# Kernel optimization log

Measured on AMD Instinct MI355X. Metric: run time of the kernel, lower is better.

The kernel has to match this reference:

```python
import jax, jax.numpy as jnp
import numpy as np

N = 50000      # nodes
E = 800000     # edges (avg degree 16)
EMB = 128      # emb_dim
NF = 7         # x_features
EF = 5         # edge_features
L = 5          # num_layer
BN_EPS = 1e-5


def setup_inputs() -> dict:
    key = jax.random.key(0)
    ks = jax.random.split(key, 12)
    s = 0.05
    return {
        "x": jax.random.normal(ks[0], (N, NF), jnp.float32),
        "edge_attr": jax.random.normal(ks[1], (E, EF), jnp.float32),
        "edge_index": jax.random.randint(ks[2], (2, E), 0, N, dtype=jnp.int32),
        "W_x": jax.random.normal(ks[3], (NF, EMB), jnp.float32) * s,
        "b_x": jax.random.normal(ks[4], (NF, EMB), jnp.float32) * s,
        "W_e": jax.random.normal(ks[5], (L, EF, EMB), jnp.float32) * s,
        "b_e": jax.random.normal(ks[6], (L, EF, EMB), jnp.float32) * s,
        # per-layer GIN update MLP: Linear(EMB,2EMB)-ReLU-Linear(2EMB,EMB)
        "W1": jax.random.normal(ks[7], (L, EMB, 2 * EMB), jnp.float32) * s,
        "b1": jnp.zeros((L, 2 * EMB), jnp.float32),
        "W2": jax.random.normal(ks[8], (L, 2 * EMB, EMB), jnp.float32) * s,
        "b2": jnp.zeros((L, EMB), jnp.float32),
        # per-layer BatchNorm1d affine params
        "gamma": jnp.ones((L, EMB), jnp.float32),
        "beta": jnp.zeros((L, EMB), jnp.float32),
    }


def reference(x, edge_attr, W_x, b_x, W_e, b_e, W1, b1, W2, b2, gamma, beta, edge_index):
    src, dst = edge_index[0], edge_index[1]
    # initial node embedding: sum of 7 Linear(1,EMB) applied per column == x @ W_x + sum(biases)
    h = x @ W_x + b_x.sum(axis=0)  # [N, EMB]
    for l in range(L):
        # edge embeddings: sum of EF Linear(1,EMB) over edge_attr columns
        e_emb = edge_attr @ W_e[l] + b_e[l].sum(axis=0)  # [E, EMB]
        sl_emb = b_e[l].sum(axis=0)  # self-loop edges have zero attr -> bias sum
        # message = x_j + edge_emb, aggr = add (scatter over dst); self loops add h + sl_emb
        msg = h[src] + e_emb                                        # [E, EMB]
        agg = jax.ops.segment_sum(msg, dst, num_segments=N) + h + sl_emb  # [N, EMB]
        # GIN update MLP
        z = jax.nn.relu(agg @ W1[l] + b1[l]) @ W2[l] + b2[l]        # [N, EMB]
        # BatchNorm1d (training-mode batch stats, biased variance)
        mu = z.mean(axis=0)
        var = z.var(axis=0)
        z = (z - mu) * jax.lax.rsqrt(var + BN_EPS) * gamma[l] + beta[l]
        # ELU on all but last layer; dropout is identity at drop_ratio=0; JK='last'
        h = jax.nn.elu(z) if l < L - 1 else z
    return h
```

## Files before the change

kernel.cpp:

```cpp
#include <hip/hip_runtime.h>
#include <math.h>

#define NN 50000
#define NE 800000
#define EMB 128
#define HID 256
#define NF 7
#define EF 5
#define NL 5
#define BN_EPS 1e-5f
#define NREP 32
#define SCAN_B 196

typedef _Float16 f16x8 __attribute__((ext_vector_type(8)));
typedef __attribute__((ext_vector_type(4))) float f32x4;

__device__ inline unsigned pkh2(float a, float b) {
    union { unsigned v; _Float16 h[2]; } x;
    x.h[0] = (_Float16)a; x.h[1] = (_Float16)b;
    return x.v;
}
__device__ inline float2 uph2(unsigned u) {
    union { unsigned v; _Float16 h[2]; } x; x.v = u;
    return make_float2((float)x.h[0], (float)x.h[1]);
}
__device__ inline unsigned short f2h_bits(float f) {
    _Float16 h = (_Float16)f;
    return __builtin_bit_cast(unsigned short, h);
}
__device__ inline float h_bits2f(unsigned short b) {
    return (float)__builtin_bit_cast(_Float16, b);
}

__global__ void k_prep(const float* __restrict__ b_x, const float* __restrict__ b_e,
                       float* __restrict__ bsum_x, float* __restrict__ bsum_e,
                       int* __restrict__ counts, int* __restrict__ cursor) {
    int tid = threadIdx.x;
    if (blockIdx.x == 0 && tid < EMB) {
        float s = 0.f;
        for (int f = 0; f < NF; ++f) s += b_x[f * EMB + tid];
        bsum_x[tid] = s;
        for (int l = 0; l < NL; ++l) {
            float se = 0.f;
            for (int f = 0; f < EF; ++f) se += b_e[(l * EF + f) * EMB + tid];
            bsum_e[l * EMB + tid] = se;
        }
    }
    int gid = blockIdx.x * blockDim.x + tid;
    int stride = gridDim.x * blockDim.x;
    for (int i = gid; i < NN; i += stride) { counts[i] = 0; cursor[i] = 0; }
}

__global__ void k_prepw(const float* __restrict__ W1, const float* __restrict__ W2,
                        unsigned short* __restrict__ W1ph, unsigned short* __restrict__ W1pl,
                        unsigned short* __restrict__ W2ph, unsigned short* __restrict__ W2pl) {
    const int TOT = NL * EMB * HID;
    int gid = blockIdx.x * blockDim.x + threadIdx.x;
    if (gid < TOT) {
        int l = gid / (EMB * HID);
        int r = gid % (EMB * HID);
        int w = r >> 13;
        int rem = r & 8191;
        int h2 = rem >> 11;
        int rem2 = rem & 2047;
        int kk = rem2 >> 9;
        int rem3 = rem2 & 511;
        int lane = rem3 >> 3;
        int j = rem3 & 7;
        int hc = w * 64 + h2 * 16 + (lane & 15);
        int k = kk * 32 + (lane >> 4) * 8 + j;
        float wv = W1[((size_t)l * EMB + k) * HID + hc];
        unsigned short hi = f2h_bits(wv);
        W1ph[gid] = hi;
        W1pl[gid] = f2h_bits(wv - h_bits2f(hi));
    } else if (gid < 2 * TOT) {
        int g = gid - TOT;
        int l = g / (EMB * HID);
        int r = g % (EMB * HID);
        int w = r >> 13;
        int rem = r & 8191;
        int o2 = rem >> 12;
        int rem2 = rem & 4095;
        int kk = rem2 >> 9;
        int rem3 = rem2 & 511;
        int lane = rem3 >> 3;
        int j = rem3 & 7;
        int oc = w * 32 + o2 * 16 + (lane & 15);
        int k2 = kk * 32 + (lane >> 4) * 8 + j;
        float wv = W2[((size_t)l * HID + k2) * EMB + oc];
        unsigned short hi = f2h_bits(wv);
        W2ph[g] = hi;
        W2pl[g] = f2h_bits(wv - h_bits2f(hi));
    }
}

__global__ void k_init(const float* __restrict__ x, const float* __restrict__ W_x,
                       const float* __restrict__ bsum_x, unsigned short* __restrict__ h16) {
    int gid = blockIdx.x * blockDim.x + threadIdx.x;
    int v = gid >> 5;
    if (v >= NN) return;
    int c = (gid & 31) << 2;
    float4 acc = *(const float4*)(bsum_x + c);
    #pragma unroll
    for (int f = 0; f < NF; ++f) {
        float xv = x[(size_t)v * NF + f];
        float4 w = *(const float4*)(W_x + f * EMB + c);
        acc.x += xv * w.x; acc.y += xv * w.y; acc.z += xv * w.z; acc.w += xv * w.w;
    }
    uint2 p = make_uint2(pkh2(acc.x, acc.y), pkh2(acc.z, acc.w));
    *(uint2*)(h16 + (size_t)v * EMB + c) = p;
}

__global__ void k_hist(const int* __restrict__ dst, int* __restrict__ counts) {
    int e = blockIdx.x * blockDim.x + threadIdx.x;
    if (e < NE) atomicAdd(&counts[dst[e]], 1);
}

__global__ void k_scan1(const int* __restrict__ counts, int* __restrict__ bsum) {
    int tid = threadIdx.x;
    int i = blockIdx.x * 256 + tid;
    int v = (i < NN) ? counts[i] : 0;
    #pragma unroll
    for (int off = 1; off < 64; off <<= 1) v += __shfl_xor(v, off, 64);
    __shared__ int ws[4];
    if ((tid & 63) == 0) ws[tid >> 6] = v;
    __syncthreads();
    if (tid == 0) bsum[blockIdx.x] = ws[0] + ws[1] + ws[2] + ws[3];
}

__global__ void k_scan2(const int* __restrict__ bsum, int* __restrict__ bpre,
                        int* __restrict__ row_start) {
    int tid = threadIdx.x;
    int x = (tid < SCAN_B) ? bsum[tid] : 0;
    int lane = tid & 63, wv = tid >> 6;
    int v = x;
    #pragma unroll
    for (int off = 1; off < 64; off <<= 1) {
        int t = __shfl_up(v, off, 64);
        if (lane >= off) v += t;
    }
    __shared__ int wsum[4];
    if (lane == 63) wsum[wv] = v;
    __syncthreads();
    int woff = 0;
    #pragma unroll
    for (int w = 0; w < 4; ++w) if (w < wv) woff += wsum[w];
    int incl = v + woff;
    if (tid < SCAN_B) bpre[tid] = incl - x;
    if (tid == 255) row_start[NN] = incl;
}

__global__ void k_scan3(const int* __restrict__ counts, const int* __restrict__ bpre,
                        int* __restrict__ row_start) {
    int tid = threadIdx.x;
    int i = blockIdx.x * 256 + tid;
    int x = (i < NN) ? counts[i] : 0;
    int lane = tid & 63, wv = tid >> 6;
    int v = x;
    #pragma unroll
    for (int off = 1; off < 64; off <<= 1) {
        int t = __shfl_up(v, off, 64);
        if (lane >= off) v += t;
    }
    __shared__ int wsum[4];
    if (lane == 63) wsum[wv] = v;
    __syncthreads();
    int woff = 0;
    #pragma unroll
    for (int w = 0; w < 4; ++w) if (w < wv) woff += wsum[w];
    if (i < NN) row_start[i] = bpre[blockIdx.x] + v + woff - x;
}

__global__ void k_fill(const int* __restrict__ src, const int* __restrict__ dst,
                       const float* __restrict__ edge_attr,
                       const int* __restrict__ row_start, int* __restrict__ cursor,
                       uint4* __restrict__ sorted_pk) {
    int e = blockIdx.x * blockDim.x + threadIdx.x;
    if (e >= NE) return;
    int d = dst[e];
    int pos = atomicAdd(&cursor[d], 1);
    int idx = row_start[d] + pos;
    const float* ea = edge_attr + (size_t)e * EF;
    float a0 = ea[0], a1 = ea[1], a2 = ea[2], a3 = ea[3], a4 = ea[4];
    uint4 pk;
    pk.x = (unsigned)src[e];
    pk.y = pkh2(a0, a1);
    pk.z = pkh2(a2, a3);
    pk.w = pkh2(a4, 0.f);
    sorted_pk[idx] = pk;
}

__global__ void k_esum(const uint4* __restrict__ sorted_pk,
                       const int* __restrict__ row_start,
                       float* __restrict__ attsum, int* __restrict__ sorted_srcc) {
    int v = blockIdx.x * blockDim.x + threadIdx.x;
    if (v >= NN) return;
    int e0 = row_start[v], e1 = row_start[v + 1];
    float s0 = 0.f, s1 = 0.f, s2 = 0.f, s3 = 0.f, s4 = 0.f;
    for (int e = e0; e < e1; ++e) {
        uint4 pk = sorted_pk[e];
        sorted_srcc[e] = (int)pk.x;
        float2 a01 = uph2(pk.y), a23 = uph2(pk.z), a4x = uph2(pk.w);
        s0 += a01.x; s1 += a01.y; s2 += a23.x; s3 += a23.y; s4 += a4x.x;
    }
    float* o = attsum + (size_t)v * 8;
    *(float4*)(o) = make_float4(s0, s1, s2, s3);
    *(float4*)(o + 4) = make_float4(s4, (float)(e1 - e0), 0.f, 0.f);
}

template<int APPLY_BN>
__global__ __launch_bounds__(256) void k_agg(
        const unsigned short* __restrict__ st16, const int* __restrict__ sorted_srcc,
        const float* __restrict__ attsum, const float* __restrict__ scsh,
        const float* __restrict__ W_e_l, const float* __restrict__ bsum_e_l,
        const int* __restrict__ row_start,
        unsigned short* __restrict__ agg16, float* __restrict__ stats) {
    int tid = threadIdx.x;
    if (blockIdx.x < NREP) stats[blockIdx.x * 2 * EMB + tid] = 0.f;
    int gid = blockIdx.x * 256 + tid;
    int v = gid >> 6;
    if (v >= NN) return;
    int c = (gid & 63) << 1;
    float2 we0 = *(const float2*)(W_e_l + 0 * EMB + c);
    float2 we1 = *(const float2*)(W_e_l + 1 * EMB + c);
    float2 we2 = *(const float2*)(W_e_l + 2 * EMB + c);
    float2 we3 = *(const float2*)(W_e_l + 3 * EMB + c);
    float2 we4 = *(const float2*)(W_e_l + 4 * EMB + c);
    float2 bs = *(const float2*)(bsum_e_l + c);
    float2 sc2 = make_float2(0.f, 0.f), sh2 = make_float2(0.f, 0.f);
    if (APPLY_BN) {
        sc2 = *(const float2*)(scsh + c);
        sh2 = *(const float2*)(scsh + EMB + c);
    }
    auto state = [&](unsigned u) -> float2 {
        float2 t = uph2(u);
        if (APPLY_BN) {
            t.x = t.x * sc2.x + sh2.x;
            t.y = t.y * sc2.y + sh2.y;
            t.x = (t.x > 0.f) ? t.x : (__expf(t.x) - 1.f);
            t.y = (t.y > 0.f) ? t.y : (__expf(t.y) - 1.f);
        }
        return t;
    };
    float2 hv = state(*(const unsigned*)(st16 + (size_t)v * EMB + c));
    const float* at = attsum + (size_t)v * 8;
    float4 a03 = *(const float4*)(at);
    float2 a45 = *(const float2*)(at + 4);
    float ax = hv.x + (a45.y + 1.f) * bs.x
             + a03.x*we0.x + a03.y*we1.x + a03.z*we2.x + a03.w*we3.x + a45.x*we4.x;
    float ay = hv.y + (a45.y + 1.f) * bs.y
             + a03.x*we0.y + a03.y*we1.y + a03.z*we2.y + a03.w*we3.y + a45.x*we4.y;
    int e0 = row_start[v], e1 = row_start[v + 1];
    int e = e0;
    for (; e + 8 <= e1; e += 8) {
        int s0 = __builtin_amdgcn_readfirstlane(sorted_srcc[e + 0]);
        int s1 = __builtin_amdgcn_readfirstlane(sorted_srcc[e + 1]);
        int s2 = __builtin_amdgcn_readfirstlane(sorted_srcc[e + 2]);
        int s3 = __builtin_amdgcn_readfirstlane(sorted_srcc[e + 3]);
        int s4 = __builtin_amdgcn_readfirstlane(sorted_srcc[e + 4]);
        int s5 = __builtin_amdgcn_readfirstlane(sorted_srcc[e + 5]);
        int s6 = __builtin_amdgcn_readfirstlane(sorted_srcc[e + 6]);
        int s7 = __builtin_amdgcn_readfirstlane(sorted_srcc[e + 7]);
        unsigned u0 = *(const unsigned*)(st16 + (size_t)s0 * EMB + c);
        unsigned u1 = *(const unsigned*)(st16 + (size_t)s1 * EMB + c);
        unsigned u2 = *(const unsigned*)(st16 + (size_t)s2 * EMB + c);
        unsigned u3 = *(const unsigned*)(st16 + (size_t)s3 * EMB + c);
        unsigned u4 = *(const unsigned*)(st16 + (size_t)s4 * EMB + c);
        unsigned u5 = *(const unsigned*)(st16 + (size_t)s5 * EMB + c);
        unsigned u6 = *(const unsigned*)(st16 + (size_t)s6 * EMB + c);
        unsigned u7 = *(const unsigned*)(st16 + (size_t)s7 * EMB + c);
        float2 h0 = state(u0), h1 = state(u1), h2 = state(u2), h3 = state(u3);
        float2 h4 = state(u4), h5 = state(u5), h6 = state(u6), h7 = state(u7);
        ax += ((h0.x + h1.x) + (h2.x + h3.x)) + ((h4.x + h5.x) + (h6.x + h7.x));
        ay += ((h0.y + h1.y) + (h2.y + h3.y)) + ((h4.y + h5.y) + (h6.y + h7.y));
    }
    for (; e < e1; ++e) {
        int s = __builtin_amdgcn_readfirstlane(sorted_srcc[e]);
        float2 hs = state(*(const unsigned*)(st16 + (size_t)s * EMB + c));
        ax += hs.x;
        ay += hs.y;
    }
    *(unsigned*)(agg16 + (size_t)v * EMB + c) = pkh2(ax, ay);
}

__global__ __launch_bounds__(256) void k_mlp(
        const unsigned short* __restrict__ agg16,
        const unsigned short* __restrict__ W1ph, const unsigned short* __restrict__ W1pl,
        const float* __restrict__ b1_l,
        const unsigned short* __restrict__ W2ph, const unsigned short* __restrict__ W2pl,
        const float* __restrict__ b2_l,
        unsigned short* __restrict__ z16, float* __restrict__ stats) {
    __shared__ unsigned short A16[32][136];
    __shared__ unsigned short Hid16[32][264];
    int tid = threadIdx.x;
    int r0 = blockIdx.x * 32;
    int rep = blockIdx.x & (NREP - 1);
    #pragma unroll
    for (int it = 0; it < 2; ++it) {
        int idx = it * 256 + tid;
        int row = idx >> 4;
        int cb = (idx & 15) * 8;
        int grow = r0 + row;
        uint4 val = make_uint4(0u, 0u, 0u, 0u);
        if (grow < NN) val = *(const uint4*)(agg16 + (size_t)grow * EMB + cb);
        *(uint4*)(&A16[row][cb]) = val;
    }
    __syncthreads();
    int wave = tid >> 6, lane = tid & 63;
    int l16 = lane & 15, quad = lane >> 4;
    {
        f16x8 af[2][4];
        #pragma unroll
        for (int nt = 0; nt < 2; ++nt)
            #pragma unroll
            for (int kk = 0; kk < 4; ++kk)
                af[nt][kk] = *(const f16x8*)(&A16[nt * 16 + l16][kk * 32 + quad * 8]);
        #pragma unroll
        for (int h2 = 0; h2 < 4; ++h2) {
            f16x8 whf[4], wlf[4];
            #pragma unroll
            for (int kk = 0; kk < 4; ++kk) {
                size_t off = ((((size_t)(wave * 4 + h2) * 4) + kk) * 64 + lane) * 8;
                whf[kk] = *(const f16x8*)(W1ph + off);
                wlf[kk] = *(const f16x8*)(W1pl + off);
            }
            float4 bv = *(const float4*)(b1_l + wave * 64 + h2 * 16 + quad * 4);
            f32x4 bias = {bv.x, bv.y, bv.z, bv.w};
            #pragma unroll
            for (int nt = 0; nt < 2; ++nt) {
                f32x4 acc = bias;
                #pragma unroll
                for (int kk = 0; kk < 4; ++kk)
                    acc = __builtin_amdgcn_mfma_f32_16x16x32_f16(whf[kk], af[nt][kk], acc, 0, 0, 0);
                #pragma unroll
                for (int kk = 0; kk < 4; ++kk)
                    acc = __builtin_amdgcn_mfma_f32_16x16x32_f16(wlf[kk], af[nt][kk], acc, 0, 0, 0);
                uint2 p;
                p.x = pkh2(fmaxf(acc[0], 0.f), fmaxf(acc[1], 0.f));
                p.y = pkh2(fmaxf(acc[2], 0.f), fmaxf(acc[3], 0.f));
                int col = wave * 64 + h2 * 16 + quad * 4;
                *(uint2*)(&Hid16[nt * 16 + l16][col]) = p;
            }
        }
    }
    __syncthreads();
    float ss[2][4] = {}, sq[2][4] = {};
    #pragma unroll
    for (int o2 = 0; o2 < 2; ++o2) {
        f16x8 w2h[8], w2l[8];
        #pragma unroll
        for (int kk = 0; kk < 8; ++kk) {
            size_t off = ((((size_t)(wave * 2 + o2) * 8) + kk) * 64 + lane) * 8;
            w2h[kk] = *(const f16x8*)(W2ph + off);
            w2l[kk] = *(const f16x8*)(W2pl + off);
        }
        float4 bv = *(const float4*)(b2_l + wave * 32 + o2 * 16 + quad * 4);
        f32x4 bias = {bv.x, bv.y, bv.z, bv.w};
        #pragma unroll
        for (int nt = 0; nt < 2; ++nt) {
            f16x8 hf[8];
            #pragma unroll
            for (int kk = 0; kk < 8; ++kk)
                hf[kk] = *(const f16x8*)(&Hid16[nt * 16 + l16][kk * 32 + quad * 8]);
            f32x4 acc = bias;
            #pragma unroll
            for (int kk = 0; kk < 8; ++kk)
                acc = __builtin_amdgcn_mfma_f32_16x16x32_f16(w2h[kk], hf[kk], acc, 0, 0, 0);
            #pragma unroll
            for (int kk = 0; kk < 8; ++kk)
                acc = __builtin_amdgcn_mfma_f32_16x16x32_f16(w2l[kk], hf[kk], acc, 0, 0, 0);
            int node = r0 + nt * 16 + l16;
            if (node < NN) {
                uint2 p = make_uint2(pkh2(acc[0], acc[1]), pkh2(acc[2], acc[3]));
                *(uint2*)(z16 + (size_t)node * EMB + wave * 32 + o2 * 16 + quad * 4) = p;
                #pragma unroll
                for (int r = 0; r < 4; ++r) {
                    ss[o2][r] += acc[r];
                    sq[o2][r] += acc[r] * acc[r];
                }
            }
        }
    }
    #pragma unroll
    for (int o2 = 0; o2 < 2; ++o2)
        #pragma unroll
        for (int r = 0; r < 4; ++r) {
            float s = ss[o2][r], q = sq[o2][r];
            #pragma unroll
            for (int m = 1; m < 16; m <<= 1) {
                s += __shfl_xor(s, m, 64);
                q += __shfl_xor(q, m, 64);
            }
            if (l16 == 0) {
                int oc = wave * 32 + o2 * 16 + quad * 4 + r;
                atomicAdd(&stats[rep * 2 * EMB + oc], s);
                atomicAdd(&stats[rep * 2 * EMB + EMB + oc], q);
            }
        }
}

__global__ void k_bnscale(const float* __restrict__ stats,
                          const float* __restrict__ gamma_l, const float* __restrict__ beta_l,
                          float* __restrict__ scsh) {
    int tid = threadIdx.x;
    float s = 0.f, q = 0.f;
    #pragma unroll
    for (int r = 0; r < NREP; ++r) {
        s += stats[r * 2 * EMB + tid];
        q += stats[r * 2 * EMB + EMB + tid];
    }
    float mu = s * (1.f / NN);
    float var = q * (1.f / NN) - mu * mu;
    float sf = gamma_l[tid] * rsqrtf(var + BN_EPS);
    scsh[tid] = sf;
    scsh[EMB + tid] = beta_l[tid] - mu * sf;
}

__global__ void k_bn(const unsigned short* __restrict__ z16, const float* __restrict__ scsh,
                     float* __restrict__ fout) {
    __shared__ float sc[EMB], sh[EMB];
    int tid = threadIdx.x;
    if (tid < EMB) {
        sc[tid] = scsh[tid];
        sh[tid] = scsh[EMB + tid];
    }
    __syncthreads();
    int gid = blockIdx.x * blockDim.x + tid;
    if (gid >= NN * EMB / 4) return;
    int c = (gid & 31) << 2;
    uint2 zp = *(const uint2*)(z16 + (size_t)gid * 4);
    float2 z01 = uph2(zp.x), z23 = uph2(zp.y);
    float o0 = z01.x * sc[c + 0] + sh[c + 0];
    float o1 = z01.y * sc[c + 1] + sh[c + 1];
    float o2 = z23.x * sc[c + 2] + sh[c + 2];
    float o3 = z23.y * sc[c + 3] + sh[c + 3];
    *(float4*)(fout + (size_t)gid * 4) = make_float4(o0, o1, o2, o3);
}

extern "C" void kernel_launch(void* const* d_in, const int* in_sizes, int n_in,
                              void* d_out, int out_size, void* d_ws, size_t ws_size,
                              hipStream_t stream) {
    const float* x         = (const float*)d_in[0];
    const float* edge_attr = (const float*)d_in[1];
    const int*   edge_idx  = (const int*)d_in[2];
    const float* W_x   = (const float*)d_in[3];
    const float* b_x   = (const float*)d_in[4];
    const float* W_e   = (const float*)d_in[5];
    const float* b_e   = (const float*)d_in[6];
    const float* W1    = (const float*)d_in[7];
    const float* b1    = (const float*)d_in[8];
    const float* W2    = (const float*)d_in[9];
    const float* b2    = (const float*)d_in[10];
    const float* gamma = (const float*)d_in[11];
    const float* beta  = (const float*)d_in[12];
    float* fout = (float*)d_out;

    const int* src = edge_idx;
    const int* dst = edge_idx + NE;

    char* p = (char*)d_ws;
    auto alloc = [&](size_t bytes) { char* q = p; p += (bytes + 255) & ~(size_t)255; return q; };
    unsigned short* h16  = (unsigned short*)alloc((size_t)NN * EMB * 2);
    unsigned short* z16  = (unsigned short*)alloc((size_t)NN * EMB * 2);
    unsigned short* agg16 = (unsigned short*)alloc((size_t)NN * EMB * 2);
    unsigned short* W1ph = (unsigned short*)alloc((size_t)NL * HID * EMB * 2);
    unsigned short* W1pl = (unsigned short*)alloc((size_t)NL * HID * EMB * 2);
    unsigned short* W2ph = (unsigned short*)alloc((size_t)NL * EMB * HID * 2);
    unsigned short* W2pl = (unsigned short*)alloc((size_t)NL * EMB * HID * 2);
    int*   row_start  = (int*)alloc((NN + 1) * sizeof(int));
    int*   counts     = (int*)alloc(NN * sizeof(int));
    int*   cursor     = (int*)alloc(NN * sizeof(int));
    uint4* sorted_pk  = (uint4*)alloc((size_t)NE * sizeof(uint4));
    int*   sorted_srcc= (int*)alloc((size_t)NE * sizeof(int));
    float* attsum     = (float*)alloc((size_t)NN * 8 * sizeof(float));
    int*   bsum       = (int*)alloc(SCAN_B * sizeof(int));
    int*   bpre       = (int*)alloc(SCAN_B * sizeof(int));
    float* stats      = (float*)alloc((size_t)NREP * 2 * EMB * sizeof(float));
    float* scsh       = (float*)alloc(2 * EMB * sizeof(float));
    float* bsum_x     = (float*)alloc(EMB * sizeof(float));
    float* bsum_e     = (float*)alloc(NL * EMB * sizeof(float));

    k_prep<<<256, 256, 0, stream>>>(b_x, b_e, bsum_x, bsum_e, counts, cursor);
    k_prepw<<<(2 * NL * EMB * HID + 255) / 256, 256, 0, stream>>>(W1, W2, W1ph, W1pl, W2ph, W2pl);
    k_init<<<(NN * 32 + 255) / 256, 256, 0, stream>>>(x, W_x, bsum_x, h16);
    k_hist<<<(NE + 255) / 256, 256, 0, stream>>>(dst, counts);
    k_scan1<<<SCAN_B, 256, 0, stream>>>(counts, bsum);
    k_scan2<<<1, 256, 0, stream>>>(bsum, bpre, row_start);
    k_scan3<<<SCAN_B, 256, 0, stream>>>(counts, bpre, row_start);
    k_fill<<<(NE + 255) / 256, 256, 0, stream>>>(src, dst, edge_attr, row_start, cursor,
                                                 sorted_pk);
    k_esum<<<SCAN_B, 256, 0, stream>>>(sorted_pk, row_start, attsum, sorted_srcc);
    const int AGG_GRID = (NN * 64 + 255) / 256;
    for (int l = 0; l < NL; ++l) {
        if (l == 0) {
            k_agg<0><<<AGG_GRID, 256, 0, stream>>>(
                h16, sorted_srcc, attsum, scsh,
                W_e + (size_t)l * EF * EMB, bsum_e + l * EMB, row_start,
                agg16, stats);
        } else {
            k_agg<1><<<AGG_GRID, 256, 0, stream>>>(
                z16, sorted_srcc, attsum, scsh,
                W_e + (size_t)l * EF * EMB, bsum_e + l * EMB, row_start,
                agg16, stats);
        }
        k_mlp<<<(NN + 31) / 32, 256, 0, stream>>>(
            agg16,
            W1ph + (size_t)l * HID * EMB, W1pl + (size_t)l * HID * EMB, b1 + (size_t)l * HID,
            W2ph + (size_t)l * EMB * HID, W2pl + (size_t)l * EMB * HID, b2 + (size_t)l * EMB,
            z16, stats);
        k_bnscale<<<1, 128, 0, stream>>>(stats, gamma + l * EMB, beta + l * EMB, scsh);
    }
    k_bn<<<(NN * EMB / 4 + 255) / 256, 256, 0, stream>>>(z16, scsh, fout);
}
```

Before: 617.7 us.

## Materialize BN+ELU state once per layer and sum neighbors in packed fp16

Instead of applying batch-norm scale/shift and ELU to every gathered neighbor in the aggregation kernel, a per-layer k_bn pass now writes the normalized, activated state to an fp16 buffer that the next aggregation gathers directly. Groups of eight neighbor rows are also summed with packed half-precision adds before being added to the fp32 accumulator. This removes redundant per-edge exp and FMA work. In exchange it adds an extra elementwise pass and extra memory traffic per layer, and it lowers accumulation precision.

```diff
diff --git a/kernel.cpp b/kernel.cpp
--- a/kernel.cpp
+++ b/kernel.cpp
@@ -13,6 +13,7 @@
 #define SCAN_B 196
 
 typedef _Float16 f16x8 __attribute__((ext_vector_type(8)));
+typedef _Float16 f16x2 __attribute__((ext_vector_type(2)));
 typedef __attribute__((ext_vector_type(4))) float f32x4;
 
 __device__ inline unsigned pkh2(float a, float b) {
@@ -31,6 +32,7 @@
 __device__ inline float h_bits2f(unsigned short b) {
     return (float)__builtin_bit_cast(_Float16, b);
 }
+__device__ inline f16x2 as_h2(unsigned u) { return __builtin_bit_cast(f16x2, u); }
 
 __global__ void k_prep(const float* __restrict__ b_x, const float* __restrict__ b_e,
                        float* __restrict__ bsum_x, float* __restrict__ bsum_e,
@@ -208,10 +210,9 @@
     *(float4*)(o + 4) = make_float4(s4, (float)(e1 - e0), 0.f, 0.f);
 }
 
-template<int APPLY_BN>
 __global__ __launch_bounds__(256) void k_agg(
-        const unsigned short* __restrict__ st16, const int* __restrict__ sorted_srcc,
-        const float* __restrict__ attsum, const float* __restrict__ scsh,
+        const unsigned short* __restrict__ h16, const int* __restrict__ sorted_srcc,
+        const float* __restrict__ attsum,
         const float* __restrict__ W_e_l, const float* __restrict__ bsum_e_l,
         const int* __restrict__ row_start,
         unsigned short* __restrict__ agg16, float* __restrict__ stats) {
@@ -227,22 +228,7 @@
     float2 we3 = *(const float2*)(W_e_l + 3 * EMB + c);
     float2 we4 = *(const float2*)(W_e_l + 4 * EMB + c);
     float2 bs = *(const float2*)(bsum_e_l + c);
-    float2 sc2 = make_float2(0.f, 0.f), sh2 = make_float2(0.f, 0.f);
-    if (APPLY_BN) {
-        sc2 = *(const float2*)(scsh + c);
-        sh2 = *(const float2*)(scsh + EMB + c);
-    }
-    auto state = [&](unsigned u) -> float2 {
-        float2 t = uph2(u);
-        if (APPLY_BN) {
-            t.x = t.x * sc2.x + sh2.x;
-            t.y = t.y * sc2.y + sh2.y;
-            t.x = (t.x > 0.f) ? t.x : (__expf(t.x) - 1.f);
-            t.y = (t.y > 0.f) ? t.y : (__expf(t.y) - 1.f);
-        }
-        return t;
-    };
-    float2 hv = state(*(const unsigned*)(st16 + (size_t)v * EMB + c));
+    float2 hv = uph2(*(const unsigned*)(h16 + (size_t)v * EMB + c));
     const float* at = attsum + (size_t)v * 8;
     float4 a03 = *(const float4*)(at);
     float2 a45 = *(const float2*)(at + 4);
@@ -261,22 +247,27 @@
         int s5 = __builtin_amdgcn_readfirstlane(sorted_srcc[e + 5]);
         int s6 = __builtin_amdgcn_readfirstlane(sorted_srcc[e + 6]);
         int s7 = __builtin_amdgcn_readfirstlane(sorted_srcc[e + 7]);
-        unsigned u0 = *(const unsigned*)(st16 + (size_t)s0 * EMB + c);
-        unsigned u1 = *(const unsigned*)(st16 + (size_t)s1 * EMB + c);
-        unsigned u2 = *(const unsigned*)(st16 + (size_t)s2 * EMB + c);
-        unsigned u3 = *(const unsigned*)(st16 + (size_t)s3 * EMB + c);
-        unsigned u4 = *(const unsigned*)(st16 + (size_t)s4 * EMB + c);
-        unsigned u5 = *(const unsigned*)(st16 + (size_t)s5 * EMB + c);
-        unsigned u6 = *(const unsigned*)(st16 + (size_t)s6 * EMB + c);
-        unsigned u7 = *(const unsigned*)(st16 + (size_t)s7 * EMB + c);
-        float2 h0 = state(u0), h1 = state(u1), h2 = state(u2), h3 = state(u3);
-        float2 h4 = state(u4), h5 = state(u5), h6 = state(u6), h7 = state(u7);
-        ax += ((h0.x + h1.x) + (h2.x + h3.x)) + ((h4.x + h5.x) + (h6.x + h7.x));
-        ay += ((h0.y + h1.y) + (h2.y + h3.y)) + ((h4.y + h5.y) + (h6.y + h7.y));
+        unsigned u0 = *(const unsigned*)(h16 + (size_t)s0 * EMB + c);
+        unsigned u1 = *(const unsigned*)(h16 + (size_t)s1 * EMB + c);
+        unsigned u2 = *(const unsigned*)(h16 + (size_t)s2 * EMB + c);
+        unsigned u3 = *(const unsigned*)(h16 + (size_t)s3 * EMB + c);
+        unsigned u4 = *(const unsigned*)(h16 + (size_t)s4 * EMB + c);
+        unsigned u5 = *(const unsigned*)(h16 + (size_t)s5 * EMB + c);
+        unsigned u6 = *(const unsigned*)(h16 + (size_t)s6 * EMB + c);
+        unsigned u7 = *(const unsigned*)(h16 + (size_t)s7 * EMB + c);
+        f16x2 p01 = as_h2(u0) + as_h2(u1);
+        f16x2 p23 = as_h2(u2) + as_h2(u3);
+        f16x2 p45 = as_h2(u4) + as_h2(u5);
+        f16x2 p67 = as_h2(u6) + as_h2(u7);
+        f16x2 p03 = p01 + p23;
+        f16x2 p47 = p45 + p67;
+        f16x2 p07 = p03 + p47;
+        ax += (float)p07.x;
+        ay += (float)p07.y;
     }
     for (; e < e1; ++e) {
         int s = __builtin_amdgcn_readfirstlane(sorted_srcc[e]);
-        float2 hs = state(*(const unsigned*)(st16 + (size_t)s * EMB + c));
+        float2 hs = uph2(*(const unsigned*)(h16 + (size_t)s * EMB + c));
         ax += hs.x;
         ay += hs.y;
     }
@@ -417,7 +408,7 @@
 }
 
 __global__ void k_bn(const unsigned short* __restrict__ z16, const float* __restrict__ scsh,
-                     float* __restrict__ fout) {
+                     unsigned short* __restrict__ h16, float* __restrict__ fout, int last) {
     __shared__ float sc[EMB], sh[EMB];
     int tid = threadIdx.x;
     if (tid < EMB) {
@@ -434,7 +425,16 @@
     float o1 = z01.y * sc[c + 1] + sh[c + 1];
     float o2 = z23.x * sc[c + 2] + sh[c + 2];
     float o3 = z23.y * sc[c + 3] + sh[c + 3];
-    *(float4*)(fout + (size_t)gid * 4) = make_float4(o0, o1, o2, o3);
+    if (!last) {
+        o0 = (o0 > 0.f) ? o0 : (__expf(o0) - 1.f);
+        o1 = (o1 > 0.f) ? o1 : (__expf(o1) - 1.f);
+        o2 = (o2 > 0.f) ? o2 : (__expf(o2) - 1.f);
+        o3 = (o3 > 0.f) ? o3 : (__expf(o3) - 1.f);
+        uint2 p = make_uint2(pkh2(o0, o1), pkh2(o2, o3));
+        *(uint2*)(h16 + (size_t)gid * 4) = p;
+    } else {
+        *(float4*)(fout + (size_t)gid * 4) = make_float4(o0, o1, o2, o3);
+    }
 }
 
 extern "C" void kernel_launch(void* const* d_in, const int* in_sizes, int n_in,
@@ -492,23 +492,17 @@
     k_esum<<<SCAN_B, 256, 0, stream>>>(sorted_pk, row_start, attsum, sorted_srcc);
     const int AGG_GRID = (NN * 64 + 255) / 256;
     for (int l = 0; l < NL; ++l) {
-        if (l == 0) {
-            k_agg<0><<<AGG_GRID, 256, 0, stream>>>(
-                h16, sorted_srcc, attsum, scsh,
-                W_e + (size_t)l * EF * EMB, bsum_e + l * EMB, row_start,
-                agg16, stats);
-        } else {
-            k_agg<1><<<AGG_GRID, 256, 0, stream>>>(
-                z16, sorted_srcc, attsum, scsh,
-                W_e + (size_t)l * EF * EMB, bsum_e + l * EMB, row_start,
-                agg16, stats);
-        }
+        k_agg<<<AGG_GRID, 256, 0, stream>>>(
+            h16, sorted_srcc, attsum,
+            W_e + (size_t)l * EF * EMB, bsum_e + l * EMB, row_start,
+            agg16, stats);
         k_mlp<<<(NN + 31) / 32, 256, 0, stream>>>(
             agg16,
             W1ph + (size_t)l * HID * EMB, W1pl + (size_t)l * HID * EMB, b1 + (size_t)l * HID,
             W2ph + (size_t)l * EMB * HID, W2pl + (size_t)l * EMB * HID, b2 + (size_t)l * EMB,
             z16, stats);
         k_bnscale<<<1, 128, 0, stream>>>(stats, gamma + l * EMB, beta + l * EMB, scsh);
-    }
-    k_bn<<<(NN * EMB / 4 + 255) / 256, 256, 0, stream>>>(z16, scsh, fout);
-}
+        k_bn<<<(NN * EMB / 4 + 255) / 256, 256, 0, stream>>>(
+            z16, scsh, h16, fout, (l == NL - 1) ? 1 : 0);
+    }
+}
```

Measured after the change: 613.6 us. About the same (-0.7%).
